# Kernel tuning notes

Hardware: AMD Instinct MI355X
Metric: run time of the kernel (lower is better)

The kernel has to match this reference:

```python
import jax, jax.numpy as jnp
import numpy as np

BS, N, H = 8, 2048, 512
NEG_INF = -1.0e9
LEAKY_SLOPE = 0.01  # torch nn.LeakyReLU default


def setup_inputs() -> dict:
    key = jax.random.key(0)
    ks = jax.random.split(key, 8)
    feats = jax.random.normal(ks[0], (BS, N, H), dtype=jnp.float32)
    # random 0/1 adjacency with self-loops so every row has >=1 neighbor
    adj = jax.random.randint(ks[1], (BS, N, N), 0, 2).astype(jnp.float32)
    adj = jnp.maximum(adj, jnp.eye(N, dtype=jnp.float32)[None])
    s = 1.0 / np.sqrt(H)
    return {
        "feats": feats,
        "adj_mat": adj,
        "fc_w": jax.random.normal(ks[2], (H, H), dtype=jnp.float32) * s,
        "fc_b": jax.random.normal(ks[3], (H,), dtype=jnp.float32) * s,
        "q_w": jax.random.normal(ks[4], (1, H), dtype=jnp.float32) * s,
        "q_b": jax.random.normal(ks[5], (1,), dtype=jnp.float32) * s,
        "k_w": jax.random.normal(ks[6], (1, H), dtype=jnp.float32) * s,
        "k_b": jax.random.normal(ks[7], (1,), dtype=jnp.float32) * s,
    }


def reference(feats, adj_mat, fc_w, fc_b, q_w, q_b, k_w, k_b):
    # feats: [bs, N, H]; torch Linear: x @ W.T + b
    feat_proj = jnp.einsum("bnh,oh->bno", feats, fc_w) + fc_b          # [bs, N, H]
    q = jnp.einsum("bnh,oh->bno", feat_proj, q_w) + q_b                # [bs, N, 1]
    k = jnp.einsum("bnh,oh->bno", feat_proj, k_w) + k_b                # [bs, N, 1]
    logits = q + jnp.swapaxes(k, 2, 1)                                 # [bs, N, N] broadcast add
    masked = logits + (1.0 - adj_mat) * NEG_INF
    masked = jnp.where(masked >= 0, masked, LEAKY_SLOPE * masked)      # LeakyReLU
    atten = jax.nn.softmax(masked, axis=-1)
    # dropout is identity in eval mode
    out = jnp.einsum("bnm,bmh->bnh", atten, feat_proj)
    return out + feats  # residual=True
```

## Files before the change

kernel.cpp:

```cpp
#include <hip/hip_runtime.h>
#include <hip/hip_bf16.h>
#include <cstdint>
#include <cstddef>

#define BSZ 8
#define NN 2048
#define HH 512
#define MROWS (BSZ * NN)
#define LOG2E 1.44269504088896f

typedef __attribute__((ext_vector_type(4))) float f32x4;
typedef __attribute__((ext_vector_type(8))) short short8;
typedef __attribute__((ext_vector_type(4))) unsigned short us4;
typedef __attribute__((ext_vector_type(2))) uint32_t u32x2;

#if __has_builtin(__builtin_amdgcn_exp2f)
#define EXP2(x) __builtin_amdgcn_exp2f(x)
#else
#define EXP2(x) __expf((x) * 0.69314718056f)
#endif

static __device__ __forceinline__ unsigned short f2bf(float f) {
    uint32_t u = __builtin_bit_cast(uint32_t, f);
    u += 0x7fffu + ((u >> 16) & 1u);
    return (unsigned short)(u >> 16);
}

static __device__ __forceinline__ void async16(const unsigned short* g, unsigned short* l) {
    __builtin_amdgcn_global_load_lds(
        (const __attribute__((address_space(1))) void*)g,
        (__attribute__((address_space(3))) void*)l, 16, 0, 0);
}

__global__ __launch_bounds__(256) void prep_kernel(
    const float* __restrict__ feats, const float* __restrict__ fc_w,
    unsigned short* __restrict__ feats_bf, unsigned short* __restrict__ fcw_bf) {
    const int bid = blockIdx.x;
    const int tid = threadIdx.x;
    if (bid < 2048) {
        const int base = bid * 1024 + tid;
#pragma unroll
        for (int j = 0; j < 4; ++j) {
            const int i = base + j * 256;
            f32x4 v = ((const f32x4*)feats)[i];
            us4 o;
#pragma unroll
            for (int c = 0; c < 4; ++c) o[c] = f2bf(v[c]);
            ((us4*)feats_bf)[i] = o;
        }
    } else {
        const int base = (bid - 2048) * 1024 + tid;
#pragma unroll
        for (int j = 0; j < 4; ++j) {
            const int i = base + j * 256;
            f32x4 v = ((const f32x4*)fc_w)[i];
            us4 o;
#pragma unroll
            for (int c = 0; c < 4; ++c) o[c] = f2bf(v[c]);
            ((us4*)fcw_bf)[i] = o;
        }
    }
}

__global__ __launch_bounds__(256) void k2_kernel(
    const unsigned short* __restrict__ A, const unsigned short* __restrict__ Bt,
    const float* __restrict__ fc_b, const float* __restrict__ q_w,
    const float* __restrict__ k_w, const float* __restrict__ adj,
    unsigned short* __restrict__ fpT, unsigned char* __restrict__ maskb,
    float* __restrict__ qpart, float* __restrict__ kpart) {
    __shared__ alignas(16) unsigned short As[2][64 * 32];
    __shared__ alignas(16) unsigned short Bs[2][128 * 32];
    __shared__ float qred[2][64], kred[2][64];
    const int bid = blockIdx.x;
    const int tid = threadIdx.x;
    const int wave = tid >> 6, lane = tid & 63;
    if (bid % 3 == 0) {
        const int g = bid / 3;
        const int wi = wave >> 1, wj = wave & 1;
        const int n0 = (g & 3) * 128;
        const int i0 = (g >> 2) * 64;
        const int K = HH;
        const int lrow = lane >> 2;
        const int lseg = (lane & 3) * 8;
        const int fro = (lane & 15) * 32 + (lane >> 4) * 8;
        f32x4 acc[2][4];
#pragma unroll
        for (int a = 0; a < 2; ++a)
#pragma unroll
            for (int c = 0; c < 4; ++c) acc[a][c] = (f32x4)(0.f);

        auto stage = [&](int buf, int k0) {
            const unsigned short* ga = A + (size_t)(i0 + wave * 16 + lrow) * K + k0 + lseg;
            async16(ga, &As[buf][(wave * 16) * 32]);
            const unsigned short* gb = Bt + (size_t)(n0 + wave * 32 + lrow) * K + k0 + lseg;
            async16(gb, &Bs[buf][(wave * 32) * 32]);
            async16(gb + (size_t)16 * K, &Bs[buf][(wave * 32 + 16) * 32]);
        };

        stage(0, 0);
        __syncthreads();

        for (int k0 = 0; k0 < K; k0 += 32) {
            const int p = (k0 >> 5) & 1;
            if (k0 + 32 < K) stage(p ^ 1, k0 + 32);
            short8 af[2], bf[4];
#pragma unroll
            for (int t = 0; t < 2; ++t) af[t] = *(const short8*)&As[p][(wi * 32 + t * 16) * 32 + fro];
#pragma unroll
            for (int t = 0; t < 4; ++t) bf[t] = *(const short8*)&Bs[p][(wj * 64 + t * 16) * 32 + fro];
#pragma unroll
            for (int it = 0; it < 2; ++it)
#pragma unroll
                for (int jt = 0; jt < 4; ++jt)
                    acc[it][jt] = __builtin_amdgcn_mfma_f32_16x16x32_bf16(af[it], bf[jt], acc[it][jt], 0, 0, 0);
            __syncthreads();
        }

        int colv[4]; float cbv[4], qwv[4], kwv[4];
#pragma unroll
        for (int jt = 0; jt < 4; ++jt) {
            colv[jt] = n0 + wj * 64 + jt * 16 + (lane & 15);
            cbv[jt] = fc_b[colv[jt]];
            qwv[jt] = q_w[colv[jt]];
            kwv[jt] = k_w[colv[jt]];
        }
        const int b = i0 >> 11;
        const int il = i0 & 2047;
#pragma unroll
        for (int jt = 0; jt < 4; ++jt) {
#pragma unroll
            for (int it = 0; it < 2; ++it) {
                const int rb = wi * 32 + it * 16 + ((lane >> 4) << 2);
                us4 o;
#pragma unroll
                for (int r = 0; r < 4; ++r) o[r] = f2bf(acc[it][jt][r] + cbv[jt]);
                *(us4*)(fpT + ((size_t)b * HH + colv[jt]) * NN + il + rb) = o;
            }
        }
#pragma unroll
        for (int it = 0; it < 2; ++it) {
#pragma unroll
            for (int r = 0; r < 4; ++r) {
                float pq = 0.f, pk = 0.f;
#pragma unroll
                for (int jt = 0; jt < 4; ++jt) {
                    float v = acc[it][jt][r] + cbv[jt];
                    pq += v * qwv[jt];
                    pk += v * kwv[jt];
                }
                for (int off = 1; off < 16; off <<= 1) {
                    pq += __shfl_xor(pq, off, 64);
                    pk += __shfl_xor(pk, off, 64);
                }
                if ((lane & 15) == 0) {
                    const int rr = wi * 32 + it * 16 + ((lane >> 4) << 2) + r;
                    qred[wj][rr] = pq;
                    kred[wj][rr] = pk;
                }
            }
        }
        __syncthreads();
        if (tid < 64) {
            const size_t o = (size_t)(n0 >> 7) * MROWS + i0 + tid;
            qpart[o] = qred[0][tid] + qred[1][tid];
            kpart[o] = kred[0][tid] + kred[1][tid];
        }
    } else {
        const int a = (bid / 3) * 2 + (bid % 3) - 1;
#pragma unroll
        for (int s = 0; s < 2; ++s) {
            const int row = a * 8 + s * 4 + wave;
            const float* ar2 = adj + (size_t)row * NN;
#pragma unroll
            for (int p = 0; p < 4; ++p) {
                f32x4 v0 = *(const f32x4*)&ar2[p * 512 + lane * 8];
                f32x4 v1 = *(const f32x4*)&ar2[p * 512 + lane * 8 + 4];
                float fb = v0[0] + 2.f * v0[1] + 4.f * v0[2] + 8.f * v0[3]
                         + 16.f * v1[0] + 32.f * v1[1] + 64.f * v1[2] + 128.f * v1[3];
                maskb[(size_t)row * 256 + p * 64 + lane] = (unsigned char)(unsigned int)fb;
            }
        }
    }
}

__global__ __launch_bounds__(512) void fused_pv_kernel(
    const unsigned short* __restrict__ fpT, const unsigned char* __restrict__ maskb,
    const float* __restrict__ qpart, const float* __restrict__ kpart,
    const float* __restrict__ q_b, const float* __restrict__ k_b,
    const float* __restrict__ feats, float* __restrict__ out) {
    __shared__ alignas(16) unsigned short As[3][64 * 32];
    __shared__ alignas(16) unsigned short Bs[3][256 * 32];
    __shared__ float kLDS[NN];
    __shared__ float qLDS[64];
    __shared__ float rzl[64];
    const int tid = threadIdx.x;
    const int wave = tid >> 6, lane = tid & 63;
    const int bid = blockIdx.x;
    const int b = bid & 7;
    const int t6 = bid >> 3;
    const int i0 = (t6 >> 1) * 64;
    const int n0 = (t6 & 1) * 256;
    const size_t rowbase = (size_t)b * NN + i0;

    {
        const float kb = k_b[0], qb = q_b[0];
#pragma unroll
        for (int s = 0; s < 4; ++s) {
            const int j = s * 512 + tid;
            const size_t gj = (size_t)b * NN + j;
            kLDS[j] = (kpart[gj] + kpart[MROWS + gj] + kpart[2 * MROWS + gj]
                     + kpart[3 * MROWS + gj] + kb) * LOG2E;
        }
        if (tid < 64) {
            const size_t gi = rowbase + tid;
            qLDS[tid] = (qpart[gi] + qpart[MROWS + gi] + qpart[2 * MROWS + gi]
                       + qpart[3 * MROWS + gi] + qb) * LOG2E;
        }
    }
    __syncthreads();

    const int r0 = tid >> 3;
    const int c4 = (tid & 7) * 4;
    const float qi = qLDS[r0];

    const unsigned short* Bt = fpT + (size_t)b * HH * NN;
    const uint32_t* mk = (const uint32_t*)maskb;
    const size_t mrow = (rowbase + r0) * 64;
    const int lrow = lane >> 2, lseg = (lane & 3) * 8;
    const int fro = (lane & 15) * 32 + (lane >> 4) * 8;

    auto stageB = [&](int buf, int k0) {
        const int rbase = wave * 32;
        const unsigned short* gb = Bt + (size_t)(n0 + rbase + lrow) * NN + k0 + lseg;
        async16(gb, &Bs[buf][rbase * 32]);
        async16(gb + (size_t)16 * NN, &Bs[buf][(rbase + 16) * 32]);
    };
    auto transform = [&](int buf, int k0, uint32_t mbits) {
        const f32x4 kv = *(const f32x4*)&kLDS[k0 + c4];
        const uint32_t nib = (mbits >> c4) & 0xfu;
        float wv[4];
#pragma unroll
        for (int c = 0; c < 4; ++c) {
            float s = qi + kv[c];
            s = fmaxf(s, 0.01f * s);
            const float e = EXP2(s);
            wv[c] = ((nib >> c) & 1u) ? e : 0.f;
        }
        u32x2 pk;
#pragma unroll
        for (int p = 0; p < 2; ++p) {
            const uint32_t lo = __builtin_bit_cast(uint32_t, wv[2 * p]);
            const uint32_t hi = __builtin_bit_cast(uint32_t, wv[2 * p + 1]);
            pk[p] = __builtin_amdgcn_perm(hi, lo, 0x07060302u);
        }
        *(u32x2*)&As[buf][r0 * 32 + c4] = pk;
    };

    f32x4 acc[4][2];
#pragma unroll
    for (int a = 0; a < 4; ++a)
#pragma unroll
        for (int c = 0; c < 2; ++c) acc[a][c] = (f32x4)(0.f);
    f32x4 acc_z[4] = {(f32x4)(0.f), (f32x4)(0.f), (f32x4)(0.f), (f32x4)(0.f)};
    short8 ones;
#pragma unroll
    for (int j = 0; j < 8; ++j) ones[j] = (short)0x3F80;

    auto compute = [&](int rd) {
        short8 af[4], bf[2];
#pragma unroll
        for (int t = 0; t < 4; ++t) af[t] = *(const short8*)&As[rd][(t * 16) * 32 + fro];
#pragma unroll
        for (int t = 0; t < 2; ++t) bf[t] = *(const short8*)&Bs[rd][(wave * 32 + t * 16) * 32 + fro];
        __builtin_amdgcn_s_setprio(1);
#pragma unroll
        for (int it = 0; it < 4; ++it)
#pragma unroll
            for (int jt = 0; jt < 2; ++jt)
                acc[it][jt] = __builtin_amdgcn_mfma_f32_16x16x32_bf16(af[it], bf[jt], acc[it][jt], 0, 0, 0);
        if (wave == 0) {
#pragma unroll
            for (int it = 0; it < 4; ++it)
                acc_z[it] = __builtin_amdgcn_mfma_f32_16x16x32_bf16(af[it], ones, acc_z[it], 0, 0, 0);
        }
        __builtin_amdgcn_s_setprio(0);
    };

    uint32_t mw_cur = mk[mrow];
    uint32_t mw_nxt = mk[mrow + 1];
    stageB(0, 0);
    transform(0, 0, mw_cur);
    asm volatile("s_waitcnt vmcnt(0)" ::: "memory");
    __builtin_amdgcn_sched_barrier(0);
    asm volatile("s_waitcnt lgkmcnt(0)" ::: "memory");
    __builtin_amdgcn_s_barrier();
    __builtin_amdgcn_sched_barrier(0);

    for (int j = 0; j < 62; ++j) {
        const int k0 = j * 32;
        const int rd = j % 3, st = (j + 1) % 3;
        uint32_t mnn;
        {
            const uint32_t* ma = mk + mrow + j + 2;
            asm volatile("global_load_dword %0, %1, off"
                         : "=v"(mnn) : "v"(ma) : "memory");
        }
        stageB(st, k0 + 32);
        asm volatile("s_waitcnt vmcnt(3)" ::: "memory");
        __builtin_amdgcn_sched_barrier(0);
        transform(st, k0 + 32, mw_nxt);
        mw_nxt = mnn;
        asm volatile("s_waitcnt lgkmcnt(0)" ::: "memory");
        __builtin_amdgcn_sched_barrier(0);
        __builtin_amdgcn_s_barrier();
        __builtin_amdgcn_sched_barrier(0);
        compute(rd);
    }
    {
        const int k0 = 62 * 32;
        stageB(0, k0 + 32);
        asm volatile("s_waitcnt vmcnt(2)" ::: "memory");
        __builtin_amdgcn_sched_barrier(0);
        transform(0, k0 + 32, mw_nxt);
        asm volatile("s_waitcnt lgkmcnt(0)" ::: "memory");
        __builtin_amdgcn_sched_barrier(0);
        __builtin_amdgcn_s_barrier();
        __builtin_amdgcn_sched_barrier(0);
        compute(62 % 3);
    }
    {
        asm volatile("s_waitcnt vmcnt(0)" ::: "memory");
        __builtin_amdgcn_sched_barrier(0);
        asm volatile("s_waitcnt lgkmcnt(0)" ::: "memory");
        __builtin_amdgcn_s_barrier();
        __builtin_amdgcn_sched_barrier(0);
        compute(0);
    }

    if (wave == 0 && (lane & 15) == 0) {
#pragma unroll
        for (int it = 0; it < 4; ++it) {
            const int rb = it * 16 + ((lane >> 4) << 2);
#pragma unroll
            for (int r = 0; r < 4; ++r) rzl[rb + r] = 1.0f / acc_z[it][r];
        }
    }
    __syncthreads();

#pragma unroll
    for (int it = 0; it < 4; ++it) {
        const int rb = it * 16 + ((lane >> 4) << 2);
        float rv[4];
#pragma unroll
        for (int r = 0; r < 4; ++r) rv[r] = rzl[rb + r];
#pragma unroll
        for (int jt = 0; jt < 2; ++jt) {
            const int col = n0 + wave * 32 + jt * 16 + (lane & 15);
#pragma unroll
            for (int r = 0; r < 4; ++r) {
                const size_t idx = (rowbase + rb + r) * HH + col;
                out[idx] = acc[it][jt][r] * rv[r] + feats[idx];
            }
        }
    }
}

extern "C" void kernel_launch(void* const* d_in, const int* in_sizes, int n_in,
                              void* d_out, int out_size, void* d_ws, size_t ws_size,
                              hipStream_t stream) {
    const float* feats = (const float*)d_in[0];
    const float* adj   = (const float*)d_in[1];
    const float* fc_w  = (const float*)d_in[2];
    const float* fc_b  = (const float*)d_in[3];
    const float* q_w   = (const float*)d_in[4];
    const float* q_b   = (const float*)d_in[5];
    const float* k_w   = (const float*)d_in[6];
    const float* k_b   = (const float*)d_in[7];
    float* out = (float*)d_out;

    char* w = (char*)d_ws;
    auto alloc = [&](size_t bytes) {
        char* p = w;
        w += (bytes + 255) & ~(size_t)255;
        return p;
    };
    unsigned short* feats_bf = (unsigned short*)alloc((size_t)BSZ * NN * HH * 2);
    unsigned short* fcw_bf   = (unsigned short*)alloc((size_t)HH * HH * 2);
    unsigned short* fpT   = (unsigned short*)alloc((size_t)BSZ * HH * NN * 2);
    unsigned char*  maskb = (unsigned char*)alloc((size_t)MROWS * 256);
    float* qpart = (float*)alloc((size_t)4 * MROWS * 4);
    float* kpart = (float*)alloc((size_t)4 * MROWS * 4);

    prep_kernel<<<2112, 256, 0, stream>>>(feats, fc_w, feats_bf, fcw_bf);
    k2_kernel<<<3072, 256, 0, stream>>>(feats_bf, fcw_bf, fc_b, q_w, k_w, adj,
                                        fpT, maskb, qpart, kpart);
    fused_pv_kernel<<<512, 512, 0, stream>>>(
        fpT, maskb, qpart, kpart, q_b, k_b, feats, out);
}
```

Baseline: 307.4 us.

## Read fp32 adjacency directly in attention kernel, drop bitmask packing pass

Removes the adjacency-to-bitmask packing blocks from the projection GEMM kernel and shrinks its grid to GEMM-only blocks. The fused attention kernel now async-stages fp32 adjacency tiles into a double-buffered LDS area and tests each element against zero when masking the exponentials. This eliminates the intermediate mask buffer and its write/read round trip. In exchange, the attention kernel reads four bytes per adjacency element instead of one bit, and each row is fetched by two column-half blocks. It also uses 16KB more LDS per block.

```diff
diff --git a/kernel.cpp b/kernel.cpp
--- a/kernel.cpp
+++ b/kernel.cpp
@@ -65,8 +65,8 @@
 __global__ __launch_bounds__(256) void k2_kernel(
     const unsigned short* __restrict__ A, const unsigned short* __restrict__ Bt,
     const float* __restrict__ fc_b, const float* __restrict__ q_w,
-    const float* __restrict__ k_w, const float* __restrict__ adj,
-    unsigned short* __restrict__ fpT, unsigned char* __restrict__ maskb,
+    const float* __restrict__ k_w,
+    unsigned short* __restrict__ fpT,
     float* __restrict__ qpart, float* __restrict__ kpart) {
     __shared__ alignas(16) unsigned short As[2][64 * 32];
     __shared__ alignas(16) unsigned short Bs[2][128 * 32];
@@ -74,122 +74,106 @@
     const int bid = blockIdx.x;
     const int tid = threadIdx.x;
     const int wave = tid >> 6, lane = tid & 63;
-    if (bid % 3 == 0) {
-        const int g = bid / 3;
-        const int wi = wave >> 1, wj = wave & 1;
-        const int n0 = (g & 3) * 128;
-        const int i0 = (g >> 2) * 64;
-        const int K = HH;
-        const int lrow = lane >> 2;
-        const int lseg = (lane & 3) * 8;
-        const int fro = (lane & 15) * 32 + (lane >> 4) * 8;
-        f32x4 acc[2][4];
-#pragma unroll
-        for (int a = 0; a < 2; ++a)
-#pragma unroll
-            for (int c = 0; c < 4; ++c) acc[a][c] = (f32x4)(0.f);
-
-        auto stage = [&](int buf, int k0) {
-            const unsigned short* ga = A + (size_t)(i0 + wave * 16 + lrow) * K + k0 + lseg;
-            async16(ga, &As[buf][(wave * 16) * 32]);
-            const unsigned short* gb = Bt + (size_t)(n0 + wave * 32 + lrow) * K + k0 + lseg;
-            async16(gb, &Bs[buf][(wave * 32) * 32]);
-            async16(gb + (size_t)16 * K, &Bs[buf][(wave * 32 + 16) * 32]);
-        };
-
-        stage(0, 0);
+    const int wi = wave >> 1, wj = wave & 1;
+    const int g = bid;
+    const int n0 = (g & 3) * 128;
+    const int i0 = (g >> 2) * 64;
+    const int K = HH;
+    const int lrow = lane >> 2;
+    const int lseg = (lane & 3) * 8;
+    const int fro = (lane & 15) * 32 + (lane >> 4) * 8;
+    f32x4 acc[2][4];
+#pragma unroll
+    for (int a = 0; a < 2; ++a)
+#pragma unroll
+        for (int c = 0; c < 4; ++c) acc[a][c] = (f32x4)(0.f);
+
+    auto stage = [&](int buf, int k0) {
+        const unsigned short* ga = A + (size_t)(i0 + wave * 16 + lrow) * K + k0 + lseg;
+        async16(ga, &As[buf][(wave * 16) * 32]);
+        const unsigned short* gb = Bt + (size_t)(n0 + wave * 32 + lrow) * K + k0 + lseg;
+        async16(gb, &Bs[buf][(wave * 32) * 32]);
+        async16(gb + (size_t)16 * K, &Bs[buf][(wave * 32 + 16) * 32]);
+    };
+
+    stage(0, 0);
+    __syncthreads();
+
+    for (int k0 = 0; k0 < K; k0 += 32) {
+        const int p = (k0 >> 5) & 1;
+        if (k0 + 32 < K) stage(p ^ 1, k0 + 32);
+        short8 af[2], bf[4];
+#pragma unroll
+        for (int t = 0; t < 2; ++t) af[t] = *(const short8*)&As[p][(wi * 32 + t * 16) * 32 + fro];
+#pragma unroll
+        for (int t = 0; t < 4; ++t) bf[t] = *(const short8*)&Bs[p][(wj * 64 + t * 16) * 32 + fro];
+#pragma unroll
+        for (int it = 0; it < 2; ++it)
+#pragma unroll
+            for (int jt = 0; jt < 4; ++jt)
+                acc[it][jt] = __builtin_amdgcn_mfma_f32_16x16x32_bf16(af[it], bf[jt], acc[it][jt], 0, 0, 0);
         __syncthreads();
-
-        for (int k0 = 0; k0 < K; k0 += 32) {
-            const int p = (k0 >> 5) & 1;
-            if (k0 + 32 < K) stage(p ^ 1, k0 + 32);
-            short8 af[2], bf[4];
-#pragma unroll
-            for (int t = 0; t < 2; ++t) af[t] = *(const short8*)&As[p][(wi * 32 + t * 16) * 32 + fro];
-#pragma unroll
-            for (int t = 0; t < 4; ++t) bf[t] = *(const short8*)&Bs[p][(wj * 64 + t * 16) * 32 + fro];
-#pragma unroll
-            for (int it = 0; it < 2; ++it)
-#pragma unroll
-                for (int jt = 0; jt < 4; ++jt)
-                    acc[it][jt] = __builtin_amdgcn_mfma_f32_16x16x32_bf16(af[it], bf[jt], acc[it][jt], 0, 0, 0);
-            __syncthreads();
-        }
-
-        int colv[4]; float cbv[4], qwv[4], kwv[4];
-#pragma unroll
-        for (int jt = 0; jt < 4; ++jt) {
-            colv[jt] = n0 + wj * 64 + jt * 16 + (lane & 15);
-            cbv[jt] = fc_b[colv[jt]];
-            qwv[jt] = q_w[colv[jt]];
-            kwv[jt] = k_w[colv[jt]];
-        }
-        const int b = i0 >> 11;
-        const int il = i0 & 2047;
-#pragma unroll
-        for (int jt = 0; jt < 4; ++jt) {
-#pragma unroll
-            for (int it = 0; it < 2; ++it) {
-                const int rb = wi * 32 + it * 16 + ((lane >> 4) << 2);
-                us4 o;
-#pragma unroll
-                for (int r = 0; r < 4; ++r) o[r] = f2bf(acc[it][jt][r] + cbv[jt]);
-                *(us4*)(fpT + ((size_t)b * HH + colv[jt]) * NN + il + rb) = o;
+    }
+
+    int colv[4]; float cbv[4], qwv[4], kwv[4];
+#pragma unroll
+    for (int jt = 0; jt < 4; ++jt) {
+        colv[jt] = n0 + wj * 64 + jt * 16 + (lane & 15);
+        cbv[jt] = fc_b[colv[jt]];
+        qwv[jt] = q_w[colv[jt]];
+        kwv[jt] = k_w[colv[jt]];
+    }
+    const int b = i0 >> 11;
+    const int il = i0 & 2047;
+#pragma unroll
+    for (int jt = 0; jt < 4; ++jt) {
+#pragma unroll
+        for (int it = 0; it < 2; ++it) {
+            const int rb = wi * 32 + it * 16 + ((lane >> 4) << 2);
+            us4 o;
+#pragma unroll
+            for (int r = 0; r < 4; ++r) o[r] = f2bf(acc[it][jt][r] + cbv[jt]);
+            *(us4*)(fpT + ((size_t)b * HH + colv[jt]) * NN + il + rb) = o;
+        }
+    }
+#pragma unroll
+    for (int it = 0; it < 2; ++it) {
+#pragma unroll
+        for (int r = 0; r < 4; ++r) {
+            float pq = 0.f, pk = 0.f;
+#pragma unroll
+            for (int jt = 0; jt < 4; ++jt) {
+                float v = acc[it][jt][r] + cbv[jt];
+                pq += v * qwv[jt];
+                pk += v * kwv[jt];
             }
-        }
-#pragma unroll
-        for (int it = 0; it < 2; ++it) {
-#pragma unroll
-            for (int r = 0; r < 4; ++r) {
-                float pq = 0.f, pk = 0.f;
-#pragma unroll
-                for (int jt = 0; jt < 4; ++jt) {
-                    float v = acc[it][jt][r] + cbv[jt];
-                    pq += v * qwv[jt];
-                    pk += v * kwv[jt];
-                }
-                for (int off = 1; off < 16; off <<= 1) {
-                    pq += __shfl_xor(pq, off, 64);
-                    pk += __shfl_xor(pk, off, 64);
-                }
-                if ((lane & 15) == 0) {
-                    const int rr = wi * 32 + it * 16 + ((lane >> 4) << 2) + r;
-                    qred[wj][rr] = pq;
-                    kred[wj][rr] = pk;
-                }
+            for (int off = 1; off < 16; off <<= 1) {
+                pq += __shfl_xor(pq, off, 64);
+                pk += __shfl_xor(pk, off, 64);
             }
-        }
-        __syncthreads();
-        if (tid < 64) {
-            const size_t o = (size_t)(n0 >> 7) * MROWS + i0 + tid;
-            qpart[o] = qred[0][tid] + qred[1][tid];
-            kpart[o] = kred[0][tid] + kred[1][tid];
-        }
-    } else {
-        const int a = (bid / 3) * 2 + (bid % 3) - 1;
-#pragma unroll
-        for (int s = 0; s < 2; ++s) {
-            const int row = a * 8 + s * 4 + wave;
-            const float* ar2 = adj + (size_t)row * NN;
-#pragma unroll
-            for (int p = 0; p < 4; ++p) {
-                f32x4 v0 = *(const f32x4*)&ar2[p * 512 + lane * 8];
-                f32x4 v1 = *(const f32x4*)&ar2[p * 512 + lane * 8 + 4];
-                float fb = v0[0] + 2.f * v0[1] + 4.f * v0[2] + 8.f * v0[3]
-                         + 16.f * v1[0] + 32.f * v1[1] + 64.f * v1[2] + 128.f * v1[3];
-                maskb[(size_t)row * 256 + p * 64 + lane] = (unsigned char)(unsigned int)fb;
+            if ((lane & 15) == 0) {
+                const int rr = wi * 32 + it * 16 + ((lane >> 4) << 2) + r;
+                qred[wj][rr] = pq;
+                kred[wj][rr] = pk;
             }
         }
     }
+    __syncthreads();
+    if (tid < 64) {
+        const size_t o = (size_t)(n0 >> 7) * MROWS + i0 + tid;
+        qpart[o] = qred[0][tid] + qred[1][tid];
+        kpart[o] = kred[0][tid] + kred[1][tid];
+    }
 }
 
 __global__ __launch_bounds__(512) void fused_pv_kernel(
-    const unsigned short* __restrict__ fpT, const unsigned char* __restrict__ maskb,
+    const unsigned short* __restrict__ fpT, const float* __restrict__ adj,
     const float* __restrict__ qpart, const float* __restrict__ kpart,
     const float* __restrict__ q_b, const float* __restrict__ k_b,
     const float* __restrict__ feats, float* __restrict__ out) {
     __shared__ alignas(16) unsigned short As[3][64 * 32];
     __shared__ alignas(16) unsigned short Bs[3][256 * 32];
+    __shared__ alignas(16) float adjS[2][64 * 32];
     __shared__ float kLDS[NN];
     __shared__ float qLDS[64];
     __shared__ float rzl[64];
@@ -224,8 +208,6 @@
     const float qi = qLDS[r0];
 
     const unsigned short* Bt = fpT + (size_t)b * HH * NN;
-    const uint32_t* mk = (const uint32_t*)maskb;
-    const size_t mrow = (rowbase + r0) * 64;
     const int lrow = lane >> 2, lseg = (lane & 3) * 8;
     const int fro = (lane & 15) * 32 + (lane >> 4) * 8;
 
@@ -235,16 +217,20 @@
         async16(gb, &Bs[buf][rbase * 32]);
         async16(gb + (size_t)16 * NN, &Bs[buf][(rbase + 16) * 32]);
     };
-    auto transform = [&](int buf, int k0, uint32_t mbits) {
+    auto stageAdj = [&](int slot, int t) {
+        const float* ga = adj + (rowbase + wave * 8 + (lane >> 3)) * NN + t * 32 + (lane & 7) * 4;
+        async16((const unsigned short*)ga, (unsigned short*)&adjS[slot][wave * 256]);
+    };
+    auto transform = [&](int buf, int slot, int k0) {
         const f32x4 kv = *(const f32x4*)&kLDS[k0 + c4];
-        const uint32_t nib = (mbits >> c4) & 0xfu;
+        const f32x4 av = *(const f32x4*)&adjS[slot][r0 * 32 + c4];
         float wv[4];
 #pragma unroll
         for (int c = 0; c < 4; ++c) {
             float s = qi + kv[c];
             s = fmaxf(s, 0.01f * s);
             const float e = EXP2(s);
-            wv[c] = ((nib >> c) & 1u) ? e : 0.f;
+            wv[c] = (av[c] != 0.f) ? e : 0.f;
         }
         u32x2 pk;
 #pragma unroll
@@ -286,30 +272,25 @@
         __builtin_amdgcn_s_setprio(0);
     };
 
-    uint32_t mw_cur = mk[mrow];
-    uint32_t mw_nxt = mk[mrow + 1];
     stageB(0, 0);
-    transform(0, 0, mw_cur);
+    stageAdj(0, 0);
+    stageAdj(1, 1);
     asm volatile("s_waitcnt vmcnt(0)" ::: "memory");
     __builtin_amdgcn_sched_barrier(0);
+    transform(0, 0, 0);
     asm volatile("s_waitcnt lgkmcnt(0)" ::: "memory");
+    __builtin_amdgcn_sched_barrier(0);
     __builtin_amdgcn_s_barrier();
     __builtin_amdgcn_sched_barrier(0);
 
     for (int j = 0; j < 62; ++j) {
         const int k0 = j * 32;
         const int rd = j % 3, st = (j + 1) % 3;
-        uint32_t mnn;
-        {
-            const uint32_t* ma = mk + mrow + j + 2;
-            asm volatile("global_load_dword %0, %1, off"
-                         : "=v"(mnn) : "v"(ma) : "memory");
-        }
         stageB(st, k0 + 32);
+        stageAdj(j & 1, j + 2);
         asm volatile("s_waitcnt vmcnt(3)" ::: "memory");
         __builtin_amdgcn_sched_barrier(0);
-        transform(st, k0 + 32, mw_nxt);
-        mw_nxt = mnn;
+        transform(st, (j + 1) & 1, k0 + 32);
         asm volatile("s_waitcnt lgkmcnt(0)" ::: "memory");
         __builtin_amdgcn_sched_barrier(0);
         __builtin_amdgcn_s_barrier();
@@ -321,7 +302,7 @@
         stageB(0, k0 + 32);
         asm volatile("s_waitcnt vmcnt(2)" ::: "memory");
         __builtin_amdgcn_sched_barrier(0);
-        transform(0, k0 + 32, mw_nxt);
+        transform(0, 1, k0 + 32);
         asm volatile("s_waitcnt lgkmcnt(0)" ::: "memory");
         __builtin_amdgcn_sched_barrier(0);
         __builtin_amdgcn_s_barrier();
@@ -387,13 +368,12 @@
     unsigned short* feats_bf = (unsigned short*)alloc((size_t)BSZ * NN * HH * 2);
     unsigned short* fcw_bf   = (unsigned short*)alloc((size_t)HH * HH * 2);
     unsigned short* fpT   = (unsigned short*)alloc((size_t)BSZ * HH * NN * 2);
-    unsigned char*  maskb = (unsigned char*)alloc((size_t)MROWS * 256);
     float* qpart = (float*)alloc((size_t)4 * MROWS * 4);
     float* kpart = (float*)alloc((size_t)4 * MROWS * 4);
 
     prep_kernel<<<2112, 256, 0, stream>>>(feats, fc_w, feats_bf, fcw_bf);
-    k2_kernel<<<3072, 256, 0, stream>>>(feats_bf, fcw_bf, fc_b, q_w, k_w, adj,
-                                        fpT, maskb, qpart, kpart);
+    k2_kernel<<<1024, 256, 0, stream>>>(feats_bf, fcw_bf, fc_b, q_w, k_w,
+                                        fpT, qpart, kpart);
     fused_pv_kernel<<<512, 512, 0, stream>>>(
-        fpT, maskb, qpart, kpart, q_b, k_b, feats, out);
-}
+        fpT, adj, qpart, kpart, q_b, k_b, feats, out);
+}
```

Result: slower. 389.4 us (+26.7%).
